# Optimization experiments

Hardware: AMD Instinct MI355X
Metric: run time of the kernel (lower is better)

## Reference

```python
import jax, jax.numpy as jnp
import numpy as np

B, S, L, E, H, T, V, D = 32, 256, 24, 300, 256, 16, 50000, 256  # batch, sents, words/sent, emb, gru_units, topics, vocab, dense


def setup_inputs() -> dict:
    key = jax.random.key(0)
    ks = jax.random.split(key, 12)
    word_ids = jax.random.randint(ks[0], (B, S, L), 0, V, dtype=jnp.int32)
    tsize = S // T
    starts = (jnp.arange(T, dtype=jnp.int32) * tsize + 1)          # 1-indexed inclusive
    ends = (jnp.arange(T, dtype=jnp.int32) * tsize + tsize)
    topic_start_ends = jnp.broadcast_to(jnp.stack([starts, ends], -1)[None], (B, T, 2))
    g = lambda k, shape, sc=0.05: (jax.random.normal(k, shape, jnp.float32) * sc)
    return {
        "word_ids": word_ids,
        "topic_start_ends": topic_start_ends,
        "emb": g(ks[1], (V, E), 0.1),
        "Wih_f": g(ks[2], (3 * H, E)), "Whh_f": g(ks[3], (3 * H, H)),
        "bih_f": jnp.zeros((3 * H,), jnp.float32), "bhh_f": jnp.zeros((3 * H,), jnp.float32),
        "Wih_b": g(ks[4], (3 * H, E)), "Whh_b": g(ks[5], (3 * H, H)),
        "bih_b": jnp.zeros((3 * H,), jnp.float32), "bhh_b": jnp.zeros((3 * H,), jnp.float32),
        "W_att": g(ks[6], (4 * H, 4 * H)), "v_att": g(ks[7], (4 * H, 1)),
        "W_dna": g(ks[8], (4 * H, D)), "b_dna": jnp.zeros((D,), jnp.float32),
        "W_out": g(ks[9], (D, 1)), "b_out": jnp.zeros((1,), jnp.float32),
    }


def _gru_dir(x, Wih, Whh, bih, bhh, reverse):
    # x: [B, S, E] -> outputs [B, S, H], final hidden [B, H]  (PyTorch GRU cell math)
    def step(h, xt):
        gi = xt @ Wih.T + bih
        gh = h @ Whh.T + bhh
        ir, iz, inn = jnp.split(gi, 3, axis=-1)
        hr, hz, hn = jnp.split(gh, 3, axis=-1)
        r = jax.nn.sigmoid(ir + hr)
        z = jax.nn.sigmoid(iz + hz)
        n = jnp.tanh(inn + r * hn)
        h2 = (1.0 - z) * n + z * h
        return h2, h2
    h0 = jnp.zeros((x.shape[0], Whh.shape[1]), x.dtype)
    hT, ys = jax.lax.scan(step, h0, jnp.swapaxes(x, 0, 1), reverse=reverse)
    return jnp.swapaxes(ys, 0, 1), hT


def _gather_seq(x, idx):
    # x: [B, S', C], idx: [B, K] -> [B, K, C]
    return jnp.take_along_axis(x, idx[:, :, None].astype(jnp.int32), axis=1)


def reference(word_ids, topic_start_ends, emb, Wih_f, Whh_f, bih_f, bhh_f,
              Wih_b, Whh_b, bih_b, bhh_b, W_att, v_att, W_dna, b_dna, W_out, b_out):
    # --- sent_encoder: per-sentence mean of word embeddings ---
    sent_vecs = jnp.mean(emb[word_ids], axis=2)  # [B, S, E]

    # --- doc_encoder: bidirectional GRU ---
    out_f, hT_f = _gru_dir(sent_vecs, Wih_f, Whh_f, bih_f, bhh_f, reverse=False)
    out_b, hT_b = _gru_dir(sent_vecs, Wih_b, Whh_b, bih_b, bhh_b, reverse=True)
    sent_rep = jnp.concatenate([out_f, out_b], axis=-1)          # [B, S, 2H]
    hidden = jnp.stack([hT_f, hT_b], axis=0)                     # [2, B, H]
    # faithful to torch: hidden.view(batch_size, 2H) (row-major reshape)
    doc_vec = hidden.reshape(B, 2 * H)
    doc_rep = jnp.broadcast_to(doc_vec[:, None, :], (B, S, 2 * H))

    # --- topic representation via boundary differencing on front/back-padded output ---
    padded = jnp.pad(sent_rep, ((0, 0), (1, 1), (0, 0)))         # [B, S+2, 2H]
    starts = topic_start_ends[..., 0]                            # [B, T], 1-indexed
    ends = topic_start_ends[..., 1]
    topic_fwd = _gather_seq(padded, ends)[..., :H] - _gather_seq(padded, starts - 1)[..., :H]
    topic_bwd = _gather_seq(padded, starts)[..., H:] - _gather_seq(padded, ends + 1)[..., H:]
    topic_mat = jnp.concatenate([topic_fwd, topic_bwd], axis=-1)  # [B, T, 2H]
    # sentence s (0-indexed) -> topic t with starts[t] <= s+1 <= ends[t]
    sent_1idx = jnp.arange(1, S + 1, dtype=jnp.int32)
    topic_id = jax.vmap(lambda e: jnp.searchsorted(e, sent_1idx, side='left'))(ends)  # [B, S]
    topic_rep = jnp.take_along_axis(topic_mat, topic_id[:, :, None], axis=1)          # [B, S, 2H]

    # --- decoder_attention ---
    cat_ds = jnp.concatenate([doc_rep, sent_rep], axis=-1)       # [B, S, 4H]
    cat_ts = jnp.concatenate([topic_rep, sent_rep], axis=-1)
    doc_scores = jnp.tanh(cat_ds @ W_att) @ v_att                # [B, S, 1]
    topic_scores = jnp.tanh(cat_ts @ W_att) @ v_att
    doc_w = jax.nn.softmax(doc_scores, axis=1)
    topic_w = jax.nn.softmax(topic_scores, axis=1)
    context = doc_w * doc_rep + topic_w * topic_rep              # [B, S, 2H]
    inp = jnp.concatenate([sent_rep, context], axis=-1)          # [B, S, 4H]
    h = jax.nn.relu(inp @ W_dna + b_dna)                         # dropout is identity (eval)
    logits = (h @ W_out + b_out)[..., 0]                         # [B, S]
    return logits
```

## Files before the change

kernel.cpp:

```cpp
#include <hip/hip_runtime.h>
#include <hip/hip_bf16.h>
#include <math.h>

#define Bd 32
#define Sd 256
#define Ld 24
#define Ed 300
#define Hd 256
#define Td 16
#define Dd 256
#define EP 320

using short8 = __attribute__((ext_vector_type(8))) short;
using f32x4  = __attribute__((ext_vector_type(4))) float;

__device__ __forceinline__ float fsigm(float x) { return 1.f / (1.f + __expf(-x)); }
__device__ __forceinline__ float ftanh(float x) {
  float e = __expf(2.f * x);
  return 1.f - 2.f / (e + 1.f);
}

__global__ void sent_means_kernel(const int* __restrict__ wids,
                                  const float* __restrict__ emb,
                                  __hip_bfloat16* __restrict__ apad) {
  int r = blockIdx.x;
  __shared__ int ids[Ld];
  int tid = threadIdx.x;
  if (tid < Ld) ids[tid] = wids[r * Ld + tid];
  __syncthreads();
  float acc = 0.f;
  if (tid < Ed) {
#pragma unroll
    for (int w = 0; w < Ld; ++w) acc += emb[(size_t)ids[w] * Ed + tid];
    acc *= (1.f / 24.f);
  }
  apad[r * EP + tid] = __float2bfloat16(tid < Ed ? acc : 0.f);
}

__global__ void prep1_kernel(const float* __restrict__ wih_f, const float* __restrict__ wih_b,
                             const float* __restrict__ whh_f, const float* __restrict__ whh_b,
                             __hip_bfloat16* __restrict__ wpadf, __hip_bfloat16* __restrict__ wpadb,
                             __hip_bfloat16* __restrict__ whhbf_f, __hip_bfloat16* __restrict__ whhbf_b) {
  int i = blockIdx.x * 512 + threadIdx.x;
  const int PW = 768 * EP;
  const int WH = 768 * Hd;
  if (i < 2 * PW) {
    const float* src = (i < PW) ? wih_f : wih_b;
    __hip_bfloat16* dst = (i < PW) ? wpadf : wpadb;
    int j = (i < PW) ? i : i - PW;
    int n = j / EP, k = j % EP;
    dst[j] = __float2bfloat16(k < Ed ? src[n * Ed + k] : 0.f);
  } else {
    int j = i - 2 * PW;
    const float* src = (j < WH) ? whh_f : whh_b;
    __hip_bfloat16* dst = (j < WH) ? whhbf_f : whhbf_b;
    int k = (j < WH) ? j : j - WH;
    dst[k] = __float2bfloat16(src[k]);
  }
}

__global__ __launch_bounds__(256) void gemm_xwt_kernel(
    const __hip_bfloat16* __restrict__ A, int lda,
    const __hip_bfloat16* __restrict__ W, int ldw,
    float* __restrict__ C, int ldc,
    int M, int N, int K,
    const float* __restrict__ bias) {
  __shared__ unsigned short la[64][32];
  __shared__ unsigned short lb[64][32];
  const int tid = threadIdx.x;
  const int m0 = blockIdx.x * 64, n0 = blockIdx.y * 64;
  const int lane = tid & 63, wid = tid >> 6;
  const int wm = (wid >> 1) * 32, wn = (wid & 1) * 32;
  const int lrow = tid >> 2, lcol = (tid & 3) * 8;
  f32x4 acc00 = {0.f, 0.f, 0.f, 0.f}, acc01 = {0.f, 0.f, 0.f, 0.f};
  f32x4 acc10 = {0.f, 0.f, 0.f, 0.f}, acc11 = {0.f, 0.f, 0.f, 0.f};
  int arow = m0 + lrow; if (arow > M - 1) arow = M - 1;
  const int brow = n0 + lrow;
  const int fr = lane & 15, fq = (lane >> 4) * 8;
  for (int k0 = 0; k0 < K; k0 += 32) {
    uint4 av = *(const uint4*)(A + (size_t)arow * lda + k0 + lcol);
    uint4 bv = *(const uint4*)(W + (size_t)brow * ldw + k0 + lcol);
    *(uint4*)(&la[lrow][lcol]) = av;
    *(uint4*)(&lb[lrow][lcol]) = bv;
    __syncthreads();
    short8 a0 = *(const short8*)(&la[wm + fr][fq]);
    short8 a1 = *(const short8*)(&la[wm + 16 + fr][fq]);
    short8 b0 = *(const short8*)(&lb[wn + fr][fq]);
    short8 b1 = *(const short8*)(&lb[wn + 16 + fr][fq]);
    acc00 = __builtin_amdgcn_mfma_f32_16x16x32_bf16(a0, b0, acc00, 0, 0, 0);
    acc01 = __builtin_amdgcn_mfma_f32_16x16x32_bf16(a0, b1, acc01, 0, 0, 0);
    acc10 = __builtin_amdgcn_mfma_f32_16x16x32_bf16(a1, b0, acc10, 0, 0, 0);
    acc11 = __builtin_amdgcn_mfma_f32_16x16x32_bf16(a1, b1, acc11, 0, 0, 0);
    __syncthreads();
  }
  const int rq = (lane >> 4) * 4;
  f32x4 accs[2][2] = {{acc00, acc01}, {acc10, acc11}};
  for (int i = 0; i < 2; ++i)
    for (int j = 0; j < 2; ++j) {
      int n = n0 + wn + j * 16 + fr;
      float bv = bias ? bias[n] : 0.f;
      for (int r2 = 0; r2 < 4; ++r2) {
        int m = m0 + wm + i * 16 + rq + r2;
        if (m < M) C[(size_t)m * ldc + n] = accs[i][j][r2] + bv;
      }
    }
}

__global__ __launch_bounds__(256) void gemm128_xwt_kernel(
    const __hip_bfloat16* __restrict__ A, int lda,
    const __hip_bfloat16* __restrict__ W, int ldw,
    float* __restrict__ C, int ldc,
    int M, int N, int K,
    const float* __restrict__ bias) {
  __shared__ unsigned short la[128][40];
  __shared__ unsigned short lb[128][40];
  const int tid = threadIdx.x;
  const int m0 = blockIdx.x * 128, n0 = blockIdx.y * 128;
  const int lane = tid & 63, wid = tid >> 6;
  const int wm = (wid >> 1) * 64, wn = (wid & 1) * 64;
  const int lrow = tid >> 2, lcol = (tid & 3) * 8;
  const int fr = lane & 15, fq = (lane >> 4) * 8;
  f32x4 acc[4][4];
#pragma unroll
  for (int i = 0; i < 4; ++i)
#pragma unroll
    for (int j = 0; j < 4; ++j) acc[i][j] = (f32x4){0.f, 0.f, 0.f, 0.f};

  for (int k0 = 0; k0 < K; k0 += 32) {
    uint4 a0 = *(const uint4*)(A + (size_t)(m0 + lrow) * lda + k0 + lcol);
    uint4 a1 = *(const uint4*)(A + (size_t)(m0 + 64 + lrow) * lda + k0 + lcol);
    uint4 b0 = *(const uint4*)(W + (size_t)(n0 + lrow) * ldw + k0 + lcol);
    uint4 b1 = *(const uint4*)(W + (size_t)(n0 + 64 + lrow) * ldw + k0 + lcol);
    *(uint4*)(&la[lrow][lcol]) = a0;
    *(uint4*)(&la[64 + lrow][lcol]) = a1;
    *(uint4*)(&lb[lrow][lcol]) = b0;
    *(uint4*)(&lb[64 + lrow][lcol]) = b1;
    __syncthreads();
    short8 af[4], bf[4];
#pragma unroll
    for (int i = 0; i < 4; ++i) af[i] = *(const short8*)(&la[wm + i * 16 + fr][fq]);
#pragma unroll
    for (int j = 0; j < 4; ++j) bf[j] = *(const short8*)(&lb[wn + j * 16 + fr][fq]);
#pragma unroll
    for (int i = 0; i < 4; ++i)
#pragma unroll
      for (int j = 0; j < 4; ++j)
        acc[i][j] = __builtin_amdgcn_mfma_f32_16x16x32_bf16(af[i], bf[j], acc[i][j], 0, 0, 0);
    __syncthreads();
  }
  const int rq = (lane >> 4) * 4;
#pragma unroll
  for (int i = 0; i < 4; ++i)
#pragma unroll
    for (int j = 0; j < 4; ++j) {
      int n = n0 + wn + j * 16 + fr;
      float bv = bias ? bias[n] : 0.f;
#pragma unroll
      for (int r2 = 0; r2 < 4; ++r2) {
        int m = m0 + wm + i * 16 + rq + r2;
        C[(size_t)m * ldc + n] = acc[i][j][r2] + bv;
      }
    }
}

__global__ __launch_bounds__(512, 1) void gru_mfma_kernel(
    const float* __restrict__ gi_f, const float* __restrict__ gi_b,
    const __hip_bfloat16* __restrict__ whhbf_f, const __hip_bfloat16* __restrict__ whhbf_b,
    const float* __restrict__ bhh_f, const float* __restrict__ bhh_b,
    float* __restrict__ sent_rep, __hip_bfloat16* __restrict__ sent_rep_bf,
    float* __restrict__ hT_f, float* __restrict__ hT_b,
    const float* __restrict__ w_att, const float* __restrict__ w_dna,
    __hip_bfloat16* __restrict__ wpack1, __hip_bfloat16* __restrict__ wpack2) {
  __shared__ float gi_lds[2][8][768];
  __shared__ __hip_bfloat16 h_bf[2][256];
  __shared__ float gh[768];
  __shared__ float stg32[2][8][256];
  const int blk = blockIdx.x;
  const int tid = threadIdx.x;

  if (blk >= 64) {
    const size_t q = (size_t)(blk - 64) * 512 + tid;
    size_t flat = q * 8;
    const size_t HALF = (size_t)1280 * 512;
    const bool second = flat >= HALF;
    size_t r = second ? flat - HALF : flat;
    int n = (int)(r >> 9), k0 = (int)(r & 511);
    __hip_bfloat16* dst = second ? wpack2 : wpack1;
#pragma unroll
    for (int j = 0; j < 8; ++j) {
      int k = k0 + j;
      float v;
      if (!second)
        v = (n < 1024) ? w_att[(size_t)k * 1024 + n]
                       : w_dna[(size_t)(512 + k) * 256 + (n - 1024)];
      else
        v = (n < 1024) ? w_att[(size_t)(512 + k) * 1024 + n]
                       : w_dna[(size_t)k * 256 + (n - 1024)];
      dst[(size_t)n * 512 + k] = __float2bfloat16(v);
    }
    return;
  }

  const int dir = blk >> 5, b = blk & 31;
  const int lane = tid & 63, w = tid >> 6;
  const float* gi = dir ? gi_b : gi_f;
  const __hip_bfloat16* whh = dir ? whhbf_b : whhbf_f;
  const float* bhh = dir ? bhh_b : bhh_f;

  {
#pragma unroll
    for (int i = 0; i < 3; ++i) {
      int idx = tid + i * 512;
      int u = idx / 192;
      int c4 = (idx - u * 192) * 4;
      int s = dir ? (255 - u) : u;
      const float* g = gi + (size_t)(((b << 8) + s) * 768 + c4);
      __builtin_amdgcn_global_load_lds(
          (const __attribute__((address_space(1))) unsigned int*)g,
          (__attribute__((address_space(3))) unsigned int*)&gi_lds[0][u][c4], 16, 0, 0);
    }
  }
  if (tid < 256) h_bf[0][tid] = __float2bfloat16(0.f);

  const int fr = lane & 15, kq = (lane >> 4) * 8;
  short8 bfrag[6][8];
  {
    const int n0 = w * 96 + fr;
#pragma unroll
    for (int nt = 0; nt < 6; ++nt)
#pragma unroll
      for (int kt = 0; kt < 8; ++kt)
        bfrag[nt][kt] = *(const short8*)(whh + (size_t)(n0 + nt * 16) * 256 + kt * 32 + kq);
  }

  float bhr = 0.f, bhz = 0.f, bhn = 0.f, hprev = 0.f;
  if (tid < 256) { bhr = bhh[tid]; bhz = bhh[256 + tid]; bhn = bhh[512 + tid]; }

  asm volatile("s_waitcnt vmcnt(0) lgkmcnt(0)\n\ts_barrier" ::: "memory");

  for (int t = 0; t < Sd; ++t) {
    const int rb = t & 1, wb = rb ^ 1;

    float gl0 = 0.f, gl1 = 0.f, gl2 = 0.f;
    if (tid < 256) {
      const float* gl = gi_lds[(t >> 3) & 1][t & 7];
      gl0 = gl[tid]; gl1 = gl[256 + tid]; gl2 = gl[512 + tid];
    }

    f32x4 acc[6];
#pragma unroll
    for (int nt = 0; nt < 6; ++nt) acc[nt] = (f32x4){0.f, 0.f, 0.f, 0.f};
#pragma unroll
    for (int kt = 0; kt < 8; ++kt) {
      short8 av = *(const short8*)(&h_bf[rb][kt * 32 + kq]);
#pragma unroll
      for (int nt = 0; nt < 6; ++nt)
        acc[nt] = __builtin_amdgcn_mfma_f32_16x16x32_bf16(av, bfrag[nt][kt], acc[nt], 0, 0, 0);
      __builtin_amdgcn_sched_group_barrier(0x100, 1, 0);
      __builtin_amdgcn_sched_group_barrier(0x008, 6, 0);
    }
    if (lane < 16) {
#pragma unroll
      for (int nt = 0; nt < 6; ++nt) gh[w * 96 + nt * 16 + lane] = acc[nt][0];
    }
    asm volatile("s_waitcnt lgkmcnt(0)\n\ts_barrier" ::: "memory");

    if (tid < 256) {
      float rr = fsigm(gl0 + gh[tid] + bhr);
      float zz = fsigm(gl1 + gh[256 + tid] + bhz);
      float nn = ftanh(gl2 + rr * (gh[512 + tid] + bhn));
      float hn = (1.f - zz) * nn + zz * hprev;
      hprev = hn;
      h_bf[wb][tid] = __float2bfloat16(hn);
      stg32[(t >> 3) & 1][t & 7][tid] = hn;
    } else if ((t & 7) == 0) {
      if (t + 8 < Sd) {
        const int buf = ((t >> 3) + 1) & 1;
#pragma unroll
        for (int i = 0; i < 6; ++i) {
          int idx = (tid - 256) + i * 256;
          int u = idx / 192;
          int c4 = (idx - u * 192) * 4;
          int s = dir ? (255 - (t + 8 + u)) : (t + 8 + u);
          const float* g = gi + (size_t)(((b << 8) + s) * 768 + c4);
          __builtin_amdgcn_global_load_lds(
              (const __attribute__((address_space(1))) unsigned int*)g,
              (__attribute__((address_space(3))) unsigned int*)&gi_lds[buf][u][c4], 16, 0, 0);
        }
      }
      if (t >= 8) {
        const int base = t - 8;
        const int gp = ((t >> 3) - 1) & 1;
        const int d = tid - 256;
#pragma unroll
        for (int u = 0; u < 8; ++u) {
          int sg = dir ? (255 - (base + u)) : (base + u);
          size_t rowg = (size_t)((b << 8) + sg);
          int col = dir ? (256 + d) : d;
          float v = stg32[gp][u][d];
          sent_rep[rowg * 512 + col] = v;
          sent_rep_bf[rowg * 512 + col] = __float2bfloat16(v);
        }
      }
    }
    if (w >= 4 && (t & 7) == 7)
      asm volatile("s_waitcnt vmcnt(0)" ::: "memory");
    asm volatile("s_waitcnt lgkmcnt(0)\n\ts_barrier" ::: "memory");
  }

  if (w >= 4) {
    const int base = 248, d = tid - 256;
#pragma unroll
    for (int u = 0; u < 8; ++u) {
      int sg = dir ? (255 - (base + u)) : (base + u);
      size_t rowg = (size_t)((b << 8) + sg);
      int col = dir ? (256 + d) : d;
      float v = stg32[1][u][d];
      sent_rep[rowg * 512 + col] = v;
      sent_rep_bf[rowg * 512 + col] = __float2bfloat16(v);
    }
  } else {
    (dir ? hT_b : hT_f)[b * 256 + tid] = hprev;
  }
}

__global__ void docvec_kernel(const float* __restrict__ hTf, const float* __restrict__ hTb,
                              __hip_bfloat16* __restrict__ dv) {
  int b = blockIdx.x, jj = threadIdx.x;
  int idx = b * 512 + jj;
  int dsel = idx >> 13;
  int rem = idx & 8191;
  int bp = rem >> 8, hp = rem & 255;
  float v = (dsel ? hTb : hTf)[bp * Hd + hp];
  dv[idx] = __float2bfloat16(v);
}

__global__ void topic_kernel(const int* __restrict__ tse, const float* __restrict__ sent_rep,
                             __hip_bfloat16* __restrict__ topic_bf) {
  int bt = blockIdx.x;
  int b = bt >> 4;
  int st = tse[bt * 2], en = tse[bt * 2 + 1];
  int dd = threadIdx.x;
  auto pad = [&](int i, int col) -> float {
    if (i < 1 || i > Sd) return 0.f;
    return sent_rep[((size_t)((b << 8) + (i - 1))) * 512 + col];
  };
  float fwd = pad(en, dd) - pad(st - 1, dd);
  float bwd = pad(st, Hd + dd) - pad(en + 1, Hd + dd);
  topic_bf[(size_t)bt * 512 + dd] = __float2bfloat16(fwd);
  topic_bf[(size_t)bt * 512 + Hd + dd] = __float2bfloat16(bwd);
}

__global__ void scores_kernel(const float* __restrict__ PD, const float* __restrict__ RT,
                              const float* __restrict__ QU, const float* __restrict__ v_att,
                              const int* __restrict__ tse,
                              float* __restrict__ dsc, float* __restrict__ tsc) {
  int r = blockIdx.x;
  int b = r >> 8, s = r & 255;
  int tid = threadIdx.x;
  int tsel = Td - 1;
  for (int t = 0; t < Td; ++t) {
    if (tse[(b * Td + t) * 2 + 1] >= s + 1) { tsel = t; break; }
  }
  const float* q = QU + (size_t)r * 1280;
  const float* p = PD + (size_t)b * 1280;
  const float* rr = RT + (size_t)(b * Td + tsel) * 1280;
  float accd = 0.f, acct = 0.f;
  for (int n = tid; n < 1024; n += 256) {
    float qv = q[n];
    float vv = v_att[n];
    accd += ftanh(p[n] + qv) * vv;
    acct += ftanh(rr[n] + qv) * vv;
  }
  __shared__ float s1[256], s2[256];
  s1[tid] = accd; s2[tid] = acct;
  __syncthreads();
  for (int off = 128; off > 0; off >>= 1) {
    if (tid < off) { s1[tid] += s1[tid + off]; s2[tid] += s2[tid + off]; }
    __syncthreads();
  }
  if (tid == 0) { dsc[r] = s1[0]; tsc[r] = s2[0]; }
}

__global__ void softmax_kernel(const float* __restrict__ dsc, const float* __restrict__ tsc,
                               float* __restrict__ dw, float* __restrict__ tw) {
  int b = blockIdx.x, s = threadIdx.x;
  __shared__ float red[256];
  for (int which = 0; which < 2; ++which) {
    const float* src = which ? tsc : dsc;
    float v = src[b * Sd + s];
    red[s] = v; __syncthreads();
    for (int off = 128; off > 0; off >>= 1) {
      if (s < off) red[s] = fmaxf(red[s], red[s + off]);
      __syncthreads();
    }
    float m = red[0]; __syncthreads();
    float e = __expf(v - m);
    red[s] = e; __syncthreads();
    for (int off = 128; off > 0; off >>= 1) {
      if (s < off) red[s] += red[s + off];
      __syncthreads();
    }
    float sum = red[0]; __syncthreads();
    (which ? tw : dw)[b * Sd + s] = e / sum;
  }
}

__global__ void final_kernel(const float* __restrict__ QU, const float* __restrict__ PD,
                             const float* __restrict__ RT, const float* __restrict__ dw,
                             const float* __restrict__ tw, const float* __restrict__ b_dna,
                             const float* __restrict__ w_out,
                             const float* __restrict__ b_out,
                             const int* __restrict__ tse, float* __restrict__ out) {
  int r = blockIdx.x;
  int b = r >> 8, s = r & 255;
  int dd = threadIdx.x;
  int tsel = Td - 1;
  for (int t = 0; t < Td; ++t) {
    if (tse[(b * Td + t) * 2 + 1] >= s + 1) { tsel = t; break; }
  }
  float wdv = dw[b * Sd + s], wtv = tw[b * Sd + s];
  float x = QU[(size_t)r * 1280 + 1024 + dd] + wdv * PD[(size_t)b * 1280 + 1024 + dd] +
            wtv * RT[(size_t)(b * Td + tsel) * 1280 + 1024 + dd] + b_dna[dd];
  x = fmaxf(x, 0.f);
  float term = x * w_out[dd];
  __shared__ float red[256];
  red[dd] = term; __syncthreads();
  for (int off = 128; off > 0; off >>= 1) {
    if (dd < off) red[dd] += red[dd + off];
    __syncthreads();
  }
  if (dd == 0) out[r] = red[0] + b_out[0];
}

static void launch_gemm(const __hip_bfloat16* A, int lda, const __hip_bfloat16* W, int ldw,
                        float* C, int ldc, int M, int N, int K,
                        const float* bias, hipStream_t stream) {
  if ((M % 128) == 0 && (N % 128) == 0) {
    dim3 grid(M / 128, N / 128);
    gemm128_xwt_kernel<<<grid, 256, 0, stream>>>(A, lda, W, ldw, C, ldc, M, N, K, bias);
  } else {
    dim3 grid((M + 63) / 64, N / 64);
    gemm_xwt_kernel<<<grid, 256, 0, stream>>>(A, lda, W, ldw, C, ldc, M, N, K, bias);
  }
}

extern "C" void kernel_launch(void* const* d_in, const int* in_sizes, int n_in,
                              void* d_out, int out_size, void* d_ws, size_t ws_size,
                              hipStream_t stream) {
  const int* word_ids = (const int*)d_in[0];
  const int* tse      = (const int*)d_in[1];
  const float* emb   = (const float*)d_in[2];
  const float* wih_f = (const float*)d_in[3];
  const float* whh_f = (const float*)d_in[4];
  const float* bih_f = (const float*)d_in[5];
  const float* bhh_f = (const float*)d_in[6];
  const float* wih_b = (const float*)d_in[7];
  const float* whh_b = (const float*)d_in[8];
  const float* bih_b = (const float*)d_in[9];
  const float* bhh_b = (const float*)d_in[10];
  const float* w_att = (const float*)d_in[11];
  const float* v_att = (const float*)d_in[12];
  const float* w_dna = (const float*)d_in[13];
  const float* b_dna = (const float*)d_in[14];
  const float* w_out = (const float*)d_in[15];
  const float* b_out = (const float*)d_in[16];
  float* out = (float*)d_out;
  char* ws = (char*)d_ws;

  const int M = Bd * Sd;

  size_t off = 0;
  auto alloc = [&](size_t sz) { size_t o = off; off += (sz + 255) & ~(size_t)255; return o; };
  size_t o_svbf   = alloc((size_t)M * EP * 2);
  size_t o_wpadf  = alloc((size_t)768 * EP * 2);
  size_t o_wpadb  = alloc((size_t)768 * EP * 2);
  size_t o_whhbf  = alloc((size_t)768 * Hd * 2 * 2);
  size_t o_wpack1 = alloc((size_t)1280 * 512 * 2);
  size_t o_wpack2 = alloc((size_t)1280 * 512 * 2);
  size_t o_hTf    = alloc((size_t)Bd * Hd * 4);
  size_t o_hTb    = alloc((size_t)Bd * Hd * 4);
  size_t o_dvbf   = alloc((size_t)Bd * 512 * 2);
  size_t o_topbf  = alloc((size_t)Bd * Td * 512 * 2);
  size_t o_PD     = alloc((size_t)Bd * 1280 * 4);
  size_t o_RT     = alloc((size_t)Bd * Td * 1280 * 4);
  size_t o_dsc    = alloc((size_t)Bd * Sd * 4);
  size_t o_tsc    = alloc((size_t)Bd * Sd * 4);
  size_t o_dw     = alloc((size_t)Bd * Sd * 4);
  size_t o_tw     = alloc((size_t)Bd * Sd * 4);
  size_t o_srep32 = alloc((size_t)M * 512 * 4);
  size_t o_srepbf = alloc((size_t)M * 512 * 2);
  size_t o_gif    = alloc((size_t)M * 768 * 4);
  size_t o_gib    = alloc((size_t)M * 768 * 4);
  size_t o_QU = o_gif;
  (void)ws_size;

  __hip_bfloat16* svbf   = (__hip_bfloat16*)(ws + o_svbf);
  __hip_bfloat16* wpadf  = (__hip_bfloat16*)(ws + o_wpadf);
  __hip_bfloat16* wpadb  = (__hip_bfloat16*)(ws + o_wpadb);
  __hip_bfloat16* whhbf_f = (__hip_bfloat16*)(ws + o_whhbf);
  __hip_bfloat16* whhbf_b = whhbf_f + 768 * Hd;
  __hip_bfloat16* wpack1 = (__hip_bfloat16*)(ws + o_wpack1);
  __hip_bfloat16* wpack2 = (__hip_bfloat16*)(ws + o_wpack2);
  float* hTf = (float*)(ws + o_hTf);
  float* hTb = (float*)(ws + o_hTb);
  __hip_bfloat16* dvbf  = (__hip_bfloat16*)(ws + o_dvbf);
  __hip_bfloat16* topbf = (__hip_bfloat16*)(ws + o_topbf);
  float* PD  = (float*)(ws + o_PD);
  float* RT  = (float*)(ws + o_RT);
  float* dsc = (float*)(ws + o_dsc);
  float* tsc = (float*)(ws + o_tsc);
  float* dw  = (float*)(ws + o_dw);
  float* tw  = (float*)(ws + o_tw);
  float* srep32 = (float*)(ws + o_srep32);
  __hip_bfloat16* srepbf = (__hip_bfloat16*)(ws + o_srepbf);
  float* gif = (float*)(ws + o_gif);
  float* gib = (float*)(ws + o_gib);
  float* QU  = (float*)(ws + o_QU);

  sent_means_kernel<<<M, EP, 0, stream>>>(word_ids, emb, svbf);
  prep1_kernel<<<1728, 512, 0, stream>>>(wih_f, wih_b, whh_f, whh_b,
                                         wpadf, wpadb, whhbf_f, whhbf_b);
  launch_gemm(svbf, EP, wpadf, EP, gif, 768, M, 768, EP, bih_f, stream);
  launch_gemm(svbf, EP, wpadb, EP, gib, 768, M, 768, EP, bih_b, stream);
  gru_mfma_kernel<<<384, 512, 0, stream>>>(gif, gib, whhbf_f, whhbf_b, bhh_f, bhh_b,
                                           srep32, srepbf, hTf, hTb,
                                           w_att, w_dna, wpack1, wpack2);
  docvec_kernel<<<Bd, 512, 0, stream>>>(hTf, hTb, dvbf);
  topic_kernel<<<Bd * Td, 256, 0, stream>>>(tse, srep32, topbf);
  launch_gemm(srepbf, 512, wpack2, 512, QU, 1280, M, 1280, 512, nullptr, stream);
  launch_gemm(dvbf, 512, wpack1, 512, PD, 1280, Bd, 1280, 512, nullptr, stream);
  launch_gemm(topbf, 512, wpack1, 512, RT, 1280, Bd * Td, 1280, 512, nullptr, stream);
  scores_kernel<<<M, 256, 0, stream>>>(PD, RT, QU, v_att, tse, dsc, tsc);
  softmax_kernel<<<Bd, 256, 0, stream>>>(dsc, tsc, dw, tw);
  final_kernel<<<M, 256, 0, stream>>>(QU, PD, RT, dw, tw, b_dna, w_out, b_out, tse, out);
}
```

Before: 583.9 us.

## Merge kernel launches: fused prep, concatenated input GEMM, grouped decoder GEMMs

Merges sentence-mean and weight-prep kernels into one launch, and merges the forward and backward input-projection GEMMs into a single GEMM with N=1536. That GEMM writes an interleaved gi buffer, and the GRU kernel now reads it with stride 1536. The docvec and topic kernels are fused into one launch, and the three decoder GEMMs (QU, RT, PD) become one grouped GEMM with 128-tile blocks, so the small-M GEMMs no longer use the 64-tile path. This cuts launch count and tail effects. The risk is that the interleaved gi layout changes GRU load locality and the PD GEMM wastes a mostly-empty 128-row tile.

```diff
diff --git a/kernel.cpp b/kernel.cpp
--- a/kernel.cpp
+++ b/kernel.cpp
@@ -20,28 +20,31 @@
   return 1.f - 2.f / (e + 1.f);
 }
 
-__global__ void sent_means_kernel(const int* __restrict__ wids,
-                                  const float* __restrict__ emb,
-                                  __hip_bfloat16* __restrict__ apad) {
-  int r = blockIdx.x;
-  __shared__ int ids[Ld];
-  int tid = threadIdx.x;
-  if (tid < Ld) ids[tid] = wids[r * Ld + tid];
-  __syncthreads();
-  float acc = 0.f;
-  if (tid < Ed) {
-#pragma unroll
-    for (int w = 0; w < Ld; ++w) acc += emb[(size_t)ids[w] * Ed + tid];
-    acc *= (1.f / 24.f);
-  }
-  apad[r * EP + tid] = __float2bfloat16(tid < Ed ? acc : 0.f);
-}
-
-__global__ void prep1_kernel(const float* __restrict__ wih_f, const float* __restrict__ wih_b,
-                             const float* __restrict__ whh_f, const float* __restrict__ whh_b,
-                             __hip_bfloat16* __restrict__ wpadf, __hip_bfloat16* __restrict__ wpadb,
-                             __hip_bfloat16* __restrict__ whhbf_f, __hip_bfloat16* __restrict__ whhbf_b) {
-  int i = blockIdx.x * 512 + threadIdx.x;
+__global__ void sentprep_kernel(const int* __restrict__ wids,
+                                const float* __restrict__ emb,
+                                __hip_bfloat16* __restrict__ apad,
+                                const float* __restrict__ wih_f, const float* __restrict__ wih_b,
+                                const float* __restrict__ whh_f, const float* __restrict__ whh_b,
+                                __hip_bfloat16* __restrict__ wpadf, __hip_bfloat16* __restrict__ wpadb,
+                                __hip_bfloat16* __restrict__ whhbf_f, __hip_bfloat16* __restrict__ whhbf_b,
+                                const float* __restrict__ bih_f, const float* __restrict__ bih_b,
+                                float* __restrict__ bias_cat) {
+  const int blk = blockIdx.x;
+  const int tid = threadIdx.x;
+  if (blk < 8192) {
+    __shared__ int ids[Ld];
+    if (tid < Ld) ids[tid] = wids[blk * Ld + tid];
+    __syncthreads();
+    float acc = 0.f;
+    if (tid < Ed) {
+#pragma unroll
+      for (int w = 0; w < Ld; ++w) acc += emb[(size_t)ids[w] * Ed + tid];
+      acc *= (1.f / 24.f);
+    }
+    apad[blk * EP + tid] = __float2bfloat16(tid < Ed ? acc : 0.f);
+    return;
+  }
+  const int i = (blk - 8192) * 320 + tid;
   const int PW = 768 * EP;
   const int WH = 768 * Hd;
   if (i < 2 * PW) {
@@ -50,60 +53,16 @@
     int j = (i < PW) ? i : i - PW;
     int n = j / EP, k = j % EP;
     dst[j] = __float2bfloat16(k < Ed ? src[n * Ed + k] : 0.f);
-  } else {
+  } else if (i < 2 * PW + 2 * WH) {
     int j = i - 2 * PW;
     const float* src = (j < WH) ? whh_f : whh_b;
     __hip_bfloat16* dst = (j < WH) ? whhbf_f : whhbf_b;
     int k = (j < WH) ? j : j - WH;
     dst[k] = __float2bfloat16(src[k]);
-  }
-}
-
-__global__ __launch_bounds__(256) void gemm_xwt_kernel(
-    const __hip_bfloat16* __restrict__ A, int lda,
-    const __hip_bfloat16* __restrict__ W, int ldw,
-    float* __restrict__ C, int ldc,
-    int M, int N, int K,
-    const float* __restrict__ bias) {
-  __shared__ unsigned short la[64][32];
-  __shared__ unsigned short lb[64][32];
-  const int tid = threadIdx.x;
-  const int m0 = blockIdx.x * 64, n0 = blockIdx.y * 64;
-  const int lane = tid & 63, wid = tid >> 6;
-  const int wm = (wid >> 1) * 32, wn = (wid & 1) * 32;
-  const int lrow = tid >> 2, lcol = (tid & 3) * 8;
-  f32x4 acc00 = {0.f, 0.f, 0.f, 0.f}, acc01 = {0.f, 0.f, 0.f, 0.f};
-  f32x4 acc10 = {0.f, 0.f, 0.f, 0.f}, acc11 = {0.f, 0.f, 0.f, 0.f};
-  int arow = m0 + lrow; if (arow > M - 1) arow = M - 1;
-  const int brow = n0 + lrow;
-  const int fr = lane & 15, fq = (lane >> 4) * 8;
-  for (int k0 = 0; k0 < K; k0 += 32) {
-    uint4 av = *(const uint4*)(A + (size_t)arow * lda + k0 + lcol);
-    uint4 bv = *(const uint4*)(W + (size_t)brow * ldw + k0 + lcol);
-    *(uint4*)(&la[lrow][lcol]) = av;
-    *(uint4*)(&lb[lrow][lcol]) = bv;
-    __syncthreads();
-    short8 a0 = *(const short8*)(&la[wm + fr][fq]);
-    short8 a1 = *(const short8*)(&la[wm + 16 + fr][fq]);
-    short8 b0 = *(const short8*)(&lb[wn + fr][fq]);
-    short8 b1 = *(const short8*)(&lb[wn + 16 + fr][fq]);
-    acc00 = __builtin_amdgcn_mfma_f32_16x16x32_bf16(a0, b0, acc00, 0, 0, 0);
-    acc01 = __builtin_amdgcn_mfma_f32_16x16x32_bf16(a0, b1, acc01, 0, 0, 0);
-    acc10 = __builtin_amdgcn_mfma_f32_16x16x32_bf16(a1, b0, acc10, 0, 0, 0);
-    acc11 = __builtin_amdgcn_mfma_f32_16x16x32_bf16(a1, b1, acc11, 0, 0, 0);
-    __syncthreads();
-  }
-  const int rq = (lane >> 4) * 4;
-  f32x4 accs[2][2] = {{acc00, acc01}, {acc10, acc11}};
-  for (int i = 0; i < 2; ++i)
-    for (int j = 0; j < 2; ++j) {
-      int n = n0 + wn + j * 16 + fr;
-      float bv = bias ? bias[n] : 0.f;
-      for (int r2 = 0; r2 < 4; ++r2) {
-        int m = m0 + wm + i * 16 + rq + r2;
-        if (m < M) C[(size_t)m * ldc + n] = accs[i][j][r2] + bv;
-      }
-    }
+  } else if (i < 2 * PW + 2 * WH + 1536) {
+    int j = i - 2 * PW - 2 * WH;
+    bias_cat[j] = (j < 768) ? bih_f[j] : bih_b[j - 768];
+  }
 }
 
 __global__ __launch_bounds__(256) void gemm128_xwt_kernel(
@@ -163,8 +122,79 @@
     }
 }
 
+__global__ __launch_bounds__(256) void gemm3_kernel(
+    const __hip_bfloat16* __restrict__ srepbf, const __hip_bfloat16* __restrict__ topbf,
+    const __hip_bfloat16* __restrict__ dvbf,
+    const __hip_bfloat16* __restrict__ wpack1, const __hip_bfloat16* __restrict__ wpack2,
+    float* __restrict__ QU, float* __restrict__ RT, float* __restrict__ PD) {
+  const int blk = blockIdx.x;
+  const __hip_bfloat16* A; const __hip_bfloat16* W; float* C;
+  int M, m0, n0;
+  if (blk < 640) {
+    A = srepbf; W = wpack2; C = QU; M = 8192;
+    m0 = (blk & 63) * 128; n0 = (blk >> 6) * 128;
+  } else if (blk < 680) {
+    int x = blk - 640;
+    A = topbf; W = wpack1; C = RT; M = 512;
+    m0 = (x & 3) * 128; n0 = (x >> 2) * 128;
+  } else {
+    int x = blk - 680;
+    A = dvbf; W = wpack1; C = PD; M = 32;
+    m0 = 0; n0 = x * 128;
+  }
+  __shared__ unsigned short la[128][40];
+  __shared__ unsigned short lb[128][40];
+  const int tid = threadIdx.x;
+  const int lane = tid & 63, wid = tid >> 6;
+  const int wm = (wid >> 1) * 64, wn = (wid & 1) * 64;
+  const int lrow = tid >> 2, lcol = (tid & 3) * 8;
+  const int fr = lane & 15, fq = (lane >> 4) * 8;
+  int ar0 = m0 + lrow;      if (ar0 > M - 1) ar0 = M - 1;
+  int ar1 = m0 + 64 + lrow; if (ar1 > M - 1) ar1 = M - 1;
+  f32x4 acc[4][4];
+#pragma unroll
+  for (int i = 0; i < 4; ++i)
+#pragma unroll
+    for (int j = 0; j < 4; ++j) acc[i][j] = (f32x4){0.f, 0.f, 0.f, 0.f};
+
+  for (int k0 = 0; k0 < 512; k0 += 32) {
+    uint4 a0 = *(const uint4*)(A + (size_t)ar0 * 512 + k0 + lcol);
+    uint4 a1 = *(const uint4*)(A + (size_t)ar1 * 512 + k0 + lcol);
+    uint4 b0 = *(const uint4*)(W + (size_t)(n0 + lrow) * 512 + k0 + lcol);
+    uint4 b1 = *(const uint4*)(W + (size_t)(n0 + 64 + lrow) * 512 + k0 + lcol);
+    *(uint4*)(&la[lrow][lcol]) = a0;
+    *(uint4*)(&la[64 + lrow][lcol]) = a1;
+    *(uint4*)(&lb[lrow][lcol]) = b0;
+    *(uint4*)(&lb[64 + lrow][lcol]) = b1;
+    __syncthreads();
+    short8 af[4], bf[4];
+#pragma unroll
+    for (int i = 0; i < 4; ++i) af[i] = *(const short8*)(&la[wm + i * 16 + fr][fq]);
+#pragma unroll
+    for (int j = 0; j < 4; ++j) bf[j] = *(const short8*)(&lb[wn + j * 16 + fr][fq]);
+#pragma unroll
+    for (int i = 0; i < 4; ++i)
+#pragma unroll
+      for (int j = 0; j < 4; ++j)
+        acc[i][j] = __builtin_amdgcn_mfma_f32_16x16x32_bf16(af[i], bf[j], acc[i][j], 0, 0, 0);
+    __syncthreads();
+  }
+  const int rq = (lane >> 4) * 4;
+#pragma unroll
+  for (int i = 0; i < 4; ++i)
+#pragma unroll
+    for (int j = 0; j < 4; ++j) {
+      int n = n0 + wn + j * 16 + fr;
+#pragma unroll
+      for (int r2 = 0; r2 < 4; ++r2) {
+        int m = m0 + wm + i * 16 + rq + r2;
+        if (m < M) C[(size_t)m * 1280 + n] = acc[i][j][r2];
+      }
+    }
+}
+
 __global__ __launch_bounds__(512, 1) void gru_mfma_kernel(
-    const float* __restrict__ gi_f, const float* __restrict__ gi_b,
+    const float* __restrict__ gi_cat,
     const __hip_bfloat16* __restrict__ whhbf_f, const __hip_bfloat16* __restrict__ whhbf_b,
     const float* __restrict__ bhh_f, const float* __restrict__ bhh_b,
     float* __restrict__ sent_rep, __hip_bfloat16* __restrict__ sent_rep_bf,
@@ -203,7 +233,7 @@
 
   const int dir = blk >> 5, b = blk & 31;
   const int lane = tid & 63, w = tid >> 6;
-  const float* gi = dir ? gi_b : gi_f;
+  const float* gi = gi_cat + (dir ? 768 : 0);
   const __hip_bfloat16* whh = dir ? whhbf_b : whhbf_f;
   const float* bhh = dir ? bhh_b : bhh_f;
 
@@ -214,7 +244,7 @@
       int u = idx / 192;
       int c4 = (idx - u * 192) * 4;
       int s = dir ? (255 - u) : u;
-      const float* g = gi + (size_t)(((b << 8) + s) * 768 + c4);
+      const float* g = gi + (size_t)((b << 8) + s) * 1536 + c4;
       __builtin_amdgcn_global_load_lds(
           (const __attribute__((address_space(1))) unsigned int*)g,
           (__attribute__((address_space(3))) unsigned int*)&gi_lds[0][u][c4], 16, 0, 0);
@@ -282,7 +312,7 @@
           int u = idx / 192;
           int c4 = (idx - u * 192) * 4;
           int s = dir ? (255 - (t + 8 + u)) : (t + 8 + u);
-          const float* g = gi + (size_t)(((b << 8) + s) * 768 + c4);
+          const float* g = gi + (size_t)((b << 8) + s) * 1536 + c4;
           __builtin_amdgcn_global_load_lds(
               (const __attribute__((address_space(1))) unsigned int*)g,
               (__attribute__((address_space(3))) unsigned int*)&gi_lds[buf][u][c4], 16, 0, 0);
@@ -324,31 +354,36 @@
   }
 }
 
-__global__ void docvec_kernel(const float* __restrict__ hTf, const float* __restrict__ hTb,
-                              __hip_bfloat16* __restrict__ dv) {
-  int b = blockIdx.x, jj = threadIdx.x;
-  int idx = b * 512 + jj;
-  int dsel = idx >> 13;
-  int rem = idx & 8191;
-  int bp = rem >> 8, hp = rem & 255;
-  float v = (dsel ? hTb : hTf)[bp * Hd + hp];
-  dv[idx] = __float2bfloat16(v);
-}
-
-__global__ void topic_kernel(const int* __restrict__ tse, const float* __restrict__ sent_rep,
-                             __hip_bfloat16* __restrict__ topic_bf) {
-  int bt = blockIdx.x;
-  int b = bt >> 4;
-  int st = tse[bt * 2], en = tse[bt * 2 + 1];
-  int dd = threadIdx.x;
-  auto pad = [&](int i, int col) -> float {
-    if (i < 1 || i > Sd) return 0.f;
-    return sent_rep[((size_t)((b << 8) + (i - 1))) * 512 + col];
-  };
-  float fwd = pad(en, dd) - pad(st - 1, dd);
-  float bwd = pad(st, Hd + dd) - pad(en + 1, Hd + dd);
-  topic_bf[(size_t)bt * 512 + dd] = __float2bfloat16(fwd);
-  topic_bf[(size_t)bt * 512 + Hd + dd] = __float2bfloat16(bwd);
+__global__ void dt_kernel(const int* __restrict__ tse, const float* __restrict__ sent_rep,
+                          const float* __restrict__ hTf, const float* __restrict__ hTb,
+                          __hip_bfloat16* __restrict__ topic_bf, __hip_bfloat16* __restrict__ dv) {
+  const int blk = blockIdx.x;
+  const int tid = threadIdx.x;
+  if (blk < 512) {
+    int bt = blk;
+    int b = bt >> 4;
+    int st = tse[bt * 2], en = tse[bt * 2 + 1];
+    auto pad = [&](int i, int col) -> float {
+      if (i < 1 || i > Sd) return 0.f;
+      return sent_rep[((size_t)((b << 8) + (i - 1))) * 512 + col];
+    };
+    float fwd = pad(en, tid) - pad(st - 1, tid);
+    float bwd = pad(st, Hd + tid) - pad(en + 1, Hd + tid);
+    topic_bf[(size_t)bt * 512 + tid] = __float2bfloat16(fwd);
+    topic_bf[(size_t)bt * 512 + Hd + tid] = __float2bfloat16(bwd);
+    return;
+  }
+  const int b = blk - 512;
+#pragma unroll
+  for (int r = 0; r < 2; ++r) {
+    int jj = tid + r * 256;
+    int idx = b * 512 + jj;
+    int dsel = idx >> 13;
+    int rem = idx & 8191;
+    int bp = rem >> 8, hp = rem & 255;
+    float v = (dsel ? hTb : hTf)[bp * Hd + hp];
+    dv[idx] = __float2bfloat16(v);
+  }
 }
 
 __global__ void scores_kernel(const float* __restrict__ PD, const float* __restrict__ RT,
@@ -431,18 +466,6 @@
     __syncthreads();
   }
   if (dd == 0) out[r] = red[0] + b_out[0];
-}
-
-static void launch_gemm(const __hip_bfloat16* A, int lda, const __hip_bfloat16* W, int ldw,
-                        float* C, int ldc, int M, int N, int K,
-                        const float* bias, hipStream_t stream) {
-  if ((M % 128) == 0 && (N % 128) == 0) {
-    dim3 grid(M / 128, N / 128);
-    gemm128_xwt_kernel<<<grid, 256, 0, stream>>>(A, lda, W, ldw, C, ldc, M, N, K, bias);
-  } else {
-    dim3 grid((M + 63) / 64, N / 64);
-    gemm_xwt_kernel<<<grid, 256, 0, stream>>>(A, lda, W, ldw, C, ldc, M, N, K, bias);
-  }
 }
 
 extern "C" void kernel_launch(void* const* d_in, const int* in_sizes, int n_in,
@@ -473,11 +496,11 @@
   size_t off = 0;
   auto alloc = [&](size_t sz) { size_t o = off; off += (sz + 255) & ~(size_t)255; return o; };
   size_t o_svbf   = alloc((size_t)M * EP * 2);
-  size_t o_wpadf  = alloc((size_t)768 * EP * 2);
-  size_t o_wpadb  = alloc((size_t)768 * EP * 2);
+  size_t o_wpad   = alloc((size_t)2 * 768 * EP * 2);
   size_t o_whhbf  = alloc((size_t)768 * Hd * 2 * 2);
   size_t o_wpack1 = alloc((size_t)1280 * 512 * 2);
   size_t o_wpack2 = alloc((size_t)1280 * 512 * 2);
+  size_t o_bcat   = alloc((size_t)1536 * 4);
   size_t o_hTf    = alloc((size_t)Bd * Hd * 4);
   size_t o_hTb    = alloc((size_t)Bd * Hd * 4);
   size_t o_dvbf   = alloc((size_t)Bd * 512 * 2);
@@ -490,18 +513,18 @@
   size_t o_tw     = alloc((size_t)Bd * Sd * 4);
   size_t o_srep32 = alloc((size_t)M * 512 * 4);
   size_t o_srepbf = alloc((size_t)M * 512 * 2);
-  size_t o_gif    = alloc((size_t)M * 768 * 4);
-  size_t o_gib    = alloc((size_t)M * 768 * 4);
-  size_t o_QU = o_gif;
+  size_t o_gicat  = alloc((size_t)M * 1536 * 4);
+  size_t o_QU = o_gicat;
   (void)ws_size;
 
   __hip_bfloat16* svbf   = (__hip_bfloat16*)(ws + o_svbf);
-  __hip_bfloat16* wpadf  = (__hip_bfloat16*)(ws + o_wpadf);
-  __hip_bfloat16* wpadb  = (__hip_bfloat16*)(ws + o_wpadb);
+  __hip_bfloat16* wpadf  = (__hip_bfloat16*)(ws + o_wpad);
+  __hip_bfloat16* wpadb  = wpadf + 768 * EP;
   __hip_bfloat16* whhbf_f = (__hip_bfloat16*)(ws + o_whhbf);
   __hip_bfloat16* whhbf_b = whhbf_f + 768 * Hd;
   __hip_bfloat16* wpack1 = (__hip_bfloat16*)(ws + o_wpack1);
   __hip_bfloat16* wpack2 = (__hip_bfloat16*)(ws + o_wpack2);
+  float* bcat = (float*)(ws + o_bcat);
   float* hTf = (float*)(ws + o_hTf);
   float* hTb = (float*)(ws + o_hTb);
   __hip_bfloat16* dvbf  = (__hip_bfloat16*)(ws + o_dvbf);
@@ -514,23 +537,23 @@
   float* tw  = (float*)(ws + o_tw);
   float* srep32 = (float*)(ws + o_srep32);
   __hip_bfloat16* srepbf = (__hip_bfloat16*)(ws + o_srepbf);
-  float* gif = (float*)(ws + o_gif);
-  float* gib = (float*)(ws + o_gib);
+  float* gicat = (float*)(ws + o_gicat);
   float* QU  = (float*)(ws + o_QU);
 
-  sent_means_kernel<<<M, EP, 0, stream>>>(word_ids, emb, svbf);
-  prep1_kernel<<<1728, 512, 0, stream>>>(wih_f, wih_b, whh_f, whh_b,
-                                         wpadf, wpadb, whhbf_f, whhbf_b);
-  launch_gemm(svbf, EP, wpadf, EP, gif, 768, M, 768, EP, bih_f, stream);
-  launch_gemm(svbf, EP, wpadb, EP, gib, 768, M, 768, EP, bih_b, stream);
-  gru_mfma_kernel<<<384, 512, 0, stream>>>(gif, gib, whhbf_f, whhbf_b, bhh_f, bhh_b,
+  sentprep_kernel<<<10962, 320, 0, stream>>>(word_ids, emb, svbf,
+                                             wih_f, wih_b, whh_f, whh_b,
+                                             wpadf, wpadb, whhbf_f, whhbf_b,
+                                             bih_f, bih_b, bcat);
+  {
+    dim3 grid(M / 128, 1536 / 128);
+    gemm128_xwt_kernel<<<grid, 256, 0, stream>>>(svbf, EP, wpadf, EP, gicat, 1536,
+                                                 M, 1536, EP, bcat);
+  }
+  gru_mfma_kernel<<<384, 512, 0, stream>>>(gicat, whhbf_f, whhbf_b, bhh_f, bhh_b,
                                            srep32, srepbf, hTf, hTb,
                                            w_att, w_dna, wpack1, wpack2);
-  docvec_kernel<<<Bd, 512, 0, stream>>>(hTf, hTb, dvbf);
-  topic_kernel<<<Bd * Td, 256, 0, stream>>>(tse, srep32, topbf);
-  launch_gemm(srepbf, 512, wpack2, 512, QU, 1280, M, 1280, 512, nullptr, stream);
-  launch_gemm(dvbf, 512, wpack1, 512, PD, 1280, Bd, 1280, 512, nullptr, stream);
-  launch_gemm(topbf, 512, wpack1, 512, RT, 1280, Bd * Td, 1280, 512, nullptr, stream);
+  dt_kernel<<<544, 256, 0, stream>>>(tse, srep32, hTf, hTb, topbf, dvbf);
+  gemm3_kernel<<<690, 256, 0, stream>>>(srepbf, topbf, dvbf, wpack1, wpack2, QU, RT, PD);
   scores_kernel<<<M, 256, 0, stream>>>(PD, RT, QU, v_att, tse, dsc, tsc);
   softmax_kernel<<<Bd, 256, 0, stream>>>(dsc, tsc, dw, tw);
   final_kernel<<<M, 256, 0, stream>>>(QU, PD, RT, dw, tw, b_dna, w_out, b_out, tse, out);
```

New measurement: 595.0 us. Within noise of the previous version (+1.9%).
